# Performance work log

Hardware: AMD Instinct MI355X
Metric: run time of the kernel (lower is better)

The kernel has to match this reference:

```python
import jax, jax.numpy as jnp
import numpy as np

LN_EPS = 1e-5  # torch LayerNorm default
K_NN = 5       # top-5 nearest patterns (simple-surprise path)


def setup_inputs() -> dict:
    key = jax.random.key(0)
    ks = jax.random.split(key, 5)
    B, S, D, M = 8, 8192, 256, 50
    return {
        "hidden_states": jax.random.normal(ks[0], (B, S, D), dtype=jnp.float32),
        "memory": jax.random.normal(ks[1], (M, D), dtype=jnp.float32),
        "W1": jax.random.normal(ks[2], (D, 2 * D), dtype=jnp.float32) * (1.0 / np.sqrt(D)),
        "b1": jnp.zeros((2 * D,), dtype=jnp.float32),
        "W2": jax.random.normal(ks[3], (2 * D, D), dtype=jnp.float32) * (1.0 / np.sqrt(2 * D)),
        "b2": jnp.zeros((D,), dtype=jnp.float32),
        "ln_gamma": jnp.ones((D,), dtype=jnp.float32),
        "ln_beta": jnp.zeros((D,), dtype=jnp.float32),
    }


def reference(hidden_states, memory, W1, b1, W2, b2, ln_gamma, ln_beta):
    # Feature extractor: Linear -> ReLU -> (Dropout, eval=identity) -> Linear -> LayerNorm
    h = jax.nn.relu(jnp.einsum("bsd,de->bse", hidden_states, W1) + b1)
    f = jnp.einsum("bse,ed->bsd", h, W2) + b2
    mu = jnp.mean(f, axis=-1, keepdims=True)
    var = jnp.var(f, axis=-1, keepdims=True)
    feats = (f - mu) * jax.lax.rsqrt(var + LN_EPS) * ln_gamma + ln_beta  # [B,S,D]

    # Simple-surprise path, vectorized over all (b, s) tokens:
    # L2 distance of each token feature to every memory pattern.
    f_sq = jnp.sum(feats * feats, axis=-1)      # [B,S]
    m_sq = jnp.sum(memory * memory, axis=-1)    # [M]
    dots = jnp.einsum("bsd,md->bsm", feats, memory)  # [B,S,M]
    d2 = jnp.maximum(f_sq[..., None] + m_sq - 2.0 * dots, 0.0)
    dists = jnp.sqrt(d2)                        # [B,S,M]

    # k smallest distances -> mean -> sigmoid(avg - 1)
    neg_knn, _ = jax.lax.top_k(-dists, K_NN)    # [B,S,K]
    avg_dist = -jnp.mean(neg_knn, axis=-1)      # [B,S]
    surprise_scores = jax.nn.sigmoid(avg_dist - 1.0)
    return surprise_scores
```

## Files before the change

### kernel.cpp

```cpp
#include <hip/hip_runtime.h>
#include <math.h>

typedef __attribute__((ext_vector_type(8))) short bf16x8;
typedef __attribute__((ext_vector_type(4))) float f32x4;
typedef unsigned short ushort_t;

static __device__ __forceinline__ unsigned short f2b(float x) {
  unsigned int u = __float_as_uint(x);
  u += 0x7FFFu + ((u >> 16) & 1u);
  return (unsigned short)(u >> 16);
}

static __device__ __forceinline__ void transpose_tile(
    const float* __restrict__ src, ushort_t* __restrict__ dst, int srcC,
    int dstC, int r0, int c0, ushort_t (*T)[72], int t) {
#pragma unroll
  for (int j = 0; j < 4; ++j) {
    int idx = j * 256 + t;
    int lr = idx >> 4;
    int lc = (idx & 15) << 2;
    float4 v = *(const float4*)(&src[(size_t)(r0 + lr) * srcC + c0 + lc]);
    T[lr][lc + 0] = f2b(v.x);
    T[lr][lc + 1] = f2b(v.y);
    T[lr][lc + 2] = f2b(v.z);
    T[lr][lc + 3] = f2b(v.w);
  }
  __syncthreads();
#pragma unroll
  for (int j = 0; j < 2; ++j) {
    int oidx = j * 256 + t;
    int lc = oidx >> 3;
    int rch = (oidx & 7) << 3;
    ushort_t tmp[8];
#pragma unroll
    for (int k = 0; k < 8; ++k) tmp[k] = T[rch + k][lc];
    *(uint4*)(&dst[(size_t)(c0 + lc) * dstC + r0 + rch]) = *(uint4*)tmp;
  }
}

__global__ void prep(const float* __restrict__ W1, const float* __restrict__ W2,
                     const float* __restrict__ mem, ushort_t* __restrict__ W1T,
                     ushort_t* __restrict__ W2T, ushort_t* __restrict__ memB,
                     float* __restrict__ msq) {
  __shared__ ushort_t T[64][72];
  int b = blockIdx.x;
  int t = threadIdx.x;
  if (b < 32) {
    int tr = b >> 3, tc = b & 7;
    transpose_tile(W1, W1T, 512, 256, tr * 64, tc * 64, T, t);
  } else if (b < 64) {
    int bb = b - 32;
    int tr = bb >> 2, tc = bb & 3;
    transpose_tile(W2, W2T, 256, 512, tr * 64, tc * 64, T, t);
  } else {
    for (int i = t; i < 16384; i += 256) {
      int r = i >> 8;
      memB[i] = (r < 50) ? f2b(mem[i]) : (ushort_t)0;
    }
    int r = t >> 2, seg = t & 3;
    float s = 0.f;
    if (r < 50) {
#pragma unroll
      for (int i = 0; i < 16; i += 4) {
        float4 v = *(const float4*)(&mem[r * 256 + seg * 64 + i * 4]);
        s += v.x * v.x + v.y * v.y + v.z * v.z + v.w * v.w;
      }
    }
    s += __shfl_xor(s, 1, 64);
    s += __shfl_xor(s, 2, 64);
    if (seg == 0) msq[r] = (r < 50) ? s : 1e30f;
  }
}

#define XP 264
#define HP 136
#define DPitch 65

__global__ __launch_bounds__(256, 3) void fused_main(
    const float* __restrict__ X, const float* __restrict__ b1v,
    const float* __restrict__ b2v, const float* __restrict__ gammav,
    const float* __restrict__ betav, const ushort_t* __restrict__ W1T,
    const ushort_t* __restrict__ W2T, const ushort_t* __restrict__ memB,
    const float* __restrict__ msq, float* __restrict__ out) {
  __shared__ __align__(16) char smem[54272];
  ushort_t* Xs = (ushort_t*)smem;
  ushort_t* Hs = (ushort_t*)(smem + 33792);
  float* distS = (float*)(smem + 33792);
  float* red = (float*)(smem + 50432);
  float* psum   = red;
  float* psumsq = red + 256;
  float* fsqp   = red + 512;
  float* muS    = red + 768;
  float* rstdS  = red + 832;
  float* fsqS   = red + 896;

  const int tid = threadIdx.x;
  const int wid = tid >> 6;
  const int lane = tid & 63;
  const int l16 = lane & 15;
  const int quad = lane >> 4;

  const float4* X4 = (const float4*)(X + (size_t)blockIdx.x * 64 * 256);
#pragma unroll
  for (int j = 0; j < 16; ++j) {
    int idx = j * 256 + tid;
    float4 v = X4[idx];
    int row = idx >> 6, c4 = (idx & 63) << 2;
    unsigned int p0 = f2b(v.x) | ((unsigned int)f2b(v.y) << 16);
    unsigned int p1 = f2b(v.z) | ((unsigned int)f2b(v.w) << 16);
    *(uint2*)(&Xs[row * XP + c4]) = make_uint2(p0, p1);
  }

  f32x4 acc2[4][4];
#pragma unroll
  for (int mt = 0; mt < 4; ++mt) {
    const float4 bb = *(const float4*)(&b2v[wid * 64 + mt * 16 + quad * 4]);
#pragma unroll
    for (int nt = 0; nt < 4; ++nt) {
      acc2[mt][nt][0] = bb.x; acc2[mt][nt][1] = bb.y;
      acc2[mt][nt][2] = bb.z; acc2[mt][nt][3] = bb.w;
    }
  }

  __syncthreads();

  for (int cc = 0; cc < 4; ++cc) {
    int hbase = cc * 128 + wid * 32;
    f32x4 acc1[2][4];
#pragma unroll
    for (int mt = 0; mt < 2; ++mt) {
      const float4 bb = *(const float4*)(&b1v[hbase + mt * 16 + quad * 4]);
#pragma unroll
      for (int nt = 0; nt < 4; ++nt) {
        acc1[mt][nt][0] = bb.x; acc1[mt][nt][1] = bb.y;
        acc1[mt][nt][2] = bb.z; acc1[mt][nt][3] = bb.w;
      }
    }
#pragma unroll
    for (int kk = 0; kk < 8; ++kk) {
      int k0 = kk * 32 + quad * 8;
      bf16x8 a[2], b[4];
#pragma unroll
      for (int mt = 0; mt < 2; ++mt)
        a[mt] = *(const bf16x8*)(W1T + (hbase + mt * 16 + l16) * 256 + k0);
#pragma unroll
      for (int nt = 0; nt < 4; ++nt)
        b[nt] = *(const bf16x8*)(Xs + (nt * 16 + l16) * XP + k0);
#pragma unroll
      for (int mt = 0; mt < 2; ++mt)
#pragma unroll
        for (int nt = 0; nt < 4; ++nt)
          acc1[mt][nt] = __builtin_amdgcn_mfma_f32_16x16x32_bf16(
              a[mt], b[nt], acc1[mt][nt], 0, 0, 0);
    }
    __syncthreads();
#pragma unroll
    for (int mt = 0; mt < 2; ++mt) {
#pragma unroll
      for (int nt = 0; nt < 4; ++nt) {
        int token = nt * 16 + l16;
        int hloc = wid * 32 + mt * 16 + quad * 4;
        f32x4 v = acc1[mt][nt];
        unsigned int p0 = f2b(fmaxf(v[0], 0.f)) | ((unsigned int)f2b(fmaxf(v[1], 0.f)) << 16);
        unsigned int p1 = f2b(fmaxf(v[2], 0.f)) | ((unsigned int)f2b(fmaxf(v[3], 0.f)) << 16);
        *(uint2*)(&Hs[token * HP + hloc]) = make_uint2(p0, p1);
      }
    }
    __syncthreads();
#pragma unroll
    for (int k2 = 0; k2 < 4; ++k2) {
      int k0 = k2 * 32 + quad * 8;
      bf16x8 a[4], b[4];
#pragma unroll
      for (int mt = 0; mt < 4; ++mt)
        a[mt] = *(const bf16x8*)(W2T + (wid * 64 + mt * 16 + l16) * 512 + cc * 128 + k0);
#pragma unroll
      for (int nt = 0; nt < 4; ++nt)
        b[nt] = *(const bf16x8*)(Hs + (nt * 16 + l16) * HP + k0);
#pragma unroll
      for (int mt = 0; mt < 4; ++mt)
#pragma unroll
        for (int nt = 0; nt < 4; ++nt)
          acc2[mt][nt] = __builtin_amdgcn_mfma_f32_16x16x32_bf16(
              a[mt], b[nt], acc2[mt][nt], 0, 0, 0);
    }
  }
  __syncthreads();

#pragma unroll
  for (int nt = 0; nt < 4; ++nt) {
    float s = 0.f, sq = 0.f;
#pragma unroll
    for (int mt = 0; mt < 4; ++mt)
#pragma unroll
      for (int r = 0; r < 4; ++r) {
        float v = acc2[mt][nt][r];
        s += v; sq += v * v;
      }
    s += __shfl_xor(s, 16, 64); sq += __shfl_xor(sq, 16, 64);
    s += __shfl_xor(s, 32, 64); sq += __shfl_xor(sq, 32, 64);
    if (quad == 0) {
      psum[wid * 64 + nt * 16 + l16] = s;
      psumsq[wid * 64 + nt * 16 + l16] = sq;
    }
  }
  __syncthreads();
  if (tid < 64) {
    float s = psum[tid] + psum[64 + tid] + psum[128 + tid] + psum[192 + tid];
    float sq = psumsq[tid] + psumsq[64 + tid] + psumsq[128 + tid] + psumsq[192 + tid];
    float mu = s * (1.f / 256.f);
    float var = sq * (1.f / 256.f) - mu * mu;
    muS[tid] = mu;
    rstdS[tid] = rsqrtf(var + 1e-5f);
  }
  __syncthreads();

  {
    float4 g[4], be[4];
#pragma unroll
    for (int mt = 0; mt < 4; ++mt) {
      g[mt]  = *(const float4*)(&gammav[wid * 64 + mt * 16 + quad * 4]);
      be[mt] = *(const float4*)(&betav[wid * 64 + mt * 16 + quad * 4]);
    }
#pragma unroll
    for (int nt = 0; nt < 4; ++nt) {
      int token = nt * 16 + l16;
      float mu = muS[token], rs = rstdS[token];
      float fs = 0.f;
#pragma unroll
      for (int mt = 0; mt < 4; ++mt) {
        float y0 = (acc2[mt][nt][0] - mu) * rs * g[mt].x + be[mt].x;
        float y1 = (acc2[mt][nt][1] - mu) * rs * g[mt].y + be[mt].y;
        float y2 = (acc2[mt][nt][2] - mu) * rs * g[mt].z + be[mt].z;
        float y3 = (acc2[mt][nt][3] - mu) * rs * g[mt].w + be[mt].w;
        fs += y0 * y0 + y1 * y1 + y2 * y2 + y3 * y3;
        unsigned int p0 = f2b(y0) | ((unsigned int)f2b(y1) << 16);
        unsigned int p1 = f2b(y2) | ((unsigned int)f2b(y3) << 16);
        *(uint2*)(&Xs[token * XP + wid * 64 + mt * 16 + quad * 4]) =
            make_uint2(p0, p1);
      }
      fs += __shfl_xor(fs, 16, 64);
      fs += __shfl_xor(fs, 32, 64);
      if (quad == 0) fsqp[wid * 64 + token] = fs;
    }
  }
  __syncthreads();

  if (tid < 64)
    fsqS[tid] = fsqp[tid] + fsqp[64 + tid] + fsqp[128 + tid] + fsqp[192 + tid];

  f32x4 acc3[4];
#pragma unroll
  for (int nt = 0; nt < 4; ++nt) {
    acc3[nt][0] = 0.f; acc3[nt][1] = 0.f; acc3[nt][2] = 0.f; acc3[nt][3] = 0.f;
  }
#pragma unroll
  for (int kk = 0; kk < 8; ++kk) {
    int k0 = kk * 32 + quad * 8;
    bf16x8 a = *(const bf16x8*)(Xs + (wid * 16 + l16) * XP + k0);
#pragma unroll
    for (int nt = 0; nt < 4; ++nt) {
      bf16x8 b = *(const bf16x8*)(memB + (nt * 16 + l16) * 256 + k0);
      acc3[nt] = __builtin_amdgcn_mfma_f32_16x16x32_bf16(a, b, acc3[nt], 0, 0, 0);
    }
  }
  __syncthreads();
  {
    float4 fsq4 = *(const float4*)(&fsqS[wid * 16 + quad * 4]);
#pragma unroll
    for (int nt = 0; nt < 4; ++nt) {
      int col = nt * 16 + l16;
      float mq = msq[col];
#pragma unroll
      for (int r = 0; r < 4; ++r) {
        float fv = (r == 0) ? fsq4.x : (r == 1) ? fsq4.y : (r == 2) ? fsq4.z : fsq4.w;
        float d2 = fv + mq - 2.f * acc3[nt][r];
        float d = sqrtf(fmaxf(d2, 0.f));
        int row = wid * 16 + quad * 4 + r;
        distS[row * DPitch + col] = d;
      }
    }
  }
  __syncthreads();

  if (tid < 64) {
    float b0 = 1e30f, b1 = 1e30f, b2 = 1e30f, b3 = 1e30f, b4 = 1e30f;
    const float* dr = &distS[tid * DPitch];
    for (int j = 0; j < 50; ++j) {
      float v = dr[j];
      b4 = fminf(b4, v);
      float t;
      if (b4 < b3) { t = b3; b3 = b4; b4 = t; }
      if (b3 < b2) { t = b2; b2 = b3; b3 = t; }
      if (b2 < b1) { t = b1; b1 = b2; b2 = t; }
      if (b1 < b0) { t = b0; b0 = b1; b1 = t; }
    }
    float avg = (b0 + b1 + b2 + b3 + b4) * 0.2f;
    float sarg = avg - 1.f;
    out[blockIdx.x * 64 + tid] = 1.f / (1.f + __expf(-sarg));
  }
}

extern "C" void kernel_launch(void* const* d_in, const int* in_sizes, int n_in,
                              void* d_out, int out_size, void* d_ws, size_t ws_size,
                              hipStream_t stream) {
  const float* X   = (const float*)d_in[0];
  const float* mem = (const float*)d_in[1];
  const float* W1  = (const float*)d_in[2];
  const float* b1  = (const float*)d_in[3];
  const float* W2  = (const float*)d_in[4];
  const float* b2  = (const float*)d_in[5];
  const float* g   = (const float*)d_in[6];
  const float* be  = (const float*)d_in[7];
  float* out = (float*)d_out;

  ushort_t* W1T  = (ushort_t*)d_ws;
  ushort_t* W2T  = W1T + 131072;
  ushort_t* memB = W2T + 131072;
  float* msq = (float*)(memB + 16384);

  prep<<<65, 256, 0, stream>>>(W1, W2, mem, W1T, W2T, memB, msq);
  fused_main<<<1024, 256, 0, stream>>>(X, b1, b2, g, be, W1T, W2T, memB, msq, out);
}
```

Before: 207.7 us.

## Halve tokens per block, swizzle LDS layout, raise occupancy to five blocks

```diff
diff --git a/kernel.cpp b/kernel.cpp
--- a/kernel.cpp
+++ b/kernel.cpp
@@ -72,27 +72,22 @@
   }
 }
 
-#define XP 264
-#define HP 136
-#define DPitch 65
-
-__global__ __launch_bounds__(256, 3) void fused_main(
+__global__ __launch_bounds__(256, 5) void fused_main(
     const float* __restrict__ X, const float* __restrict__ b1v,
     const float* __restrict__ b2v, const float* __restrict__ gammav,
     const float* __restrict__ betav, const ushort_t* __restrict__ W1T,
     const ushort_t* __restrict__ W2T, const ushort_t* __restrict__ memB,
     const float* __restrict__ msq, float* __restrict__ out) {
-  __shared__ __align__(16) char smem[54272];
-  ushort_t* Xs = (ushort_t*)smem;
-  ushort_t* Hs = (ushort_t*)(smem + 33792);
-  float* distS = (float*)(smem + 33792);
-  float* red = (float*)(smem + 50432);
-  float* psum   = red;
-  float* psumsq = red + 256;
-  float* fsqp   = red + 512;
-  float* muS    = red + 768;
-  float* rstdS  = red + 832;
-  float* fsqS   = red + 896;
+  __shared__ __align__(16) char smem[25600];
+  char* Xs = smem;
+  char* Hs = smem + 16384;
+  float* distS  = (float*)(smem + 16384);
+  float* psum   = (float*)(smem + 16384);
+  float* psumsq = (float*)(smem + 16896);
+  float* fsqp   = (float*)(smem + 24704);
+  float* muS    = (float*)(smem + 25216);
+  float* rstdS  = (float*)(smem + 25344);
+  float* fsqS   = (float*)(smem + 25472);
 
   const int tid = threadIdx.x;
   const int wid = tid >> 6;
@@ -100,23 +95,26 @@
   const int l16 = lane & 15;
   const int quad = lane >> 4;
 
-  const float4* X4 = (const float4*)(X + (size_t)blockIdx.x * 64 * 256);
-#pragma unroll
-  for (int j = 0; j < 16; ++j) {
+  const float4* X4 = (const float4*)(X + (size_t)blockIdx.x * 32 * 256);
+#pragma unroll
+  for (int j = 0; j < 8; ++j) {
     int idx = j * 256 + tid;
     float4 v = X4[idx];
-    int row = idx >> 6, c4 = (idx & 63) << 2;
+    int row = idx >> 6;
+    int c = (idx & 63) >> 1;
+    int half = idx & 1;
+    int slot = c ^ (row & 7);
     unsigned int p0 = f2b(v.x) | ((unsigned int)f2b(v.y) << 16);
     unsigned int p1 = f2b(v.z) | ((unsigned int)f2b(v.w) << 16);
-    *(uint2*)(&Xs[row * XP + c4]) = make_uint2(p0, p1);
-  }
-
-  f32x4 acc2[4][4];
+    *(uint2*)(Xs + row * 512 + slot * 16 + half * 8) = make_uint2(p0, p1);
+  }
+
+  f32x4 acc2[4][2];
 #pragma unroll
   for (int mt = 0; mt < 4; ++mt) {
     const float4 bb = *(const float4*)(&b2v[wid * 64 + mt * 16 + quad * 4]);
 #pragma unroll
-    for (int nt = 0; nt < 4; ++nt) {
+    for (int nt = 0; nt < 2; ++nt) {
       acc2[mt][nt][0] = bb.x; acc2[mt][nt][1] = bb.y;
       acc2[mt][nt][2] = bb.z; acc2[mt][nt][3] = bb.w;
     }
@@ -126,12 +124,12 @@
 
   for (int cc = 0; cc < 4; ++cc) {
     int hbase = cc * 128 + wid * 32;
-    f32x4 acc1[2][4];
+    f32x4 acc1[2][2];
 #pragma unroll
     for (int mt = 0; mt < 2; ++mt) {
       const float4 bb = *(const float4*)(&b1v[hbase + mt * 16 + quad * 4]);
 #pragma unroll
-      for (int nt = 0; nt < 4; ++nt) {
+      for (int nt = 0; nt < 2; ++nt) {
         acc1[mt][nt][0] = bb.x; acc1[mt][nt][1] = bb.y;
         acc1[mt][nt][2] = bb.z; acc1[mt][nt][3] = bb.w;
       }
@@ -139,17 +137,20 @@
 #pragma unroll
     for (int kk = 0; kk < 8; ++kk) {
       int k0 = kk * 32 + quad * 8;
-      bf16x8 a[2], b[4];
+      bf16x8 a[2], b[2];
 #pragma unroll
       for (int mt = 0; mt < 2; ++mt)
         a[mt] = *(const bf16x8*)(W1T + (hbase + mt * 16 + l16) * 256 + k0);
-#pragma unroll
-      for (int nt = 0; nt < 4; ++nt)
-        b[nt] = *(const bf16x8*)(Xs + (nt * 16 + l16) * XP + k0);
+      int c = kk * 4 + quad;
+#pragma unroll
+      for (int nt = 0; nt < 2; ++nt) {
+        int t = nt * 16 + l16;
+        b[nt] = *(const bf16x8*)(Xs + t * 512 + (c ^ (t & 7)) * 16);
+      }
 #pragma unroll
       for (int mt = 0; mt < 2; ++mt)
 #pragma unroll
-        for (int nt = 0; nt < 4; ++nt)
+        for (int nt = 0; nt < 2; ++nt)
           acc1[mt][nt] = __builtin_amdgcn_mfma_f32_16x16x32_bf16(
               a[mt], b[nt], acc1[mt][nt], 0, 0, 0);
     }
@@ -157,30 +158,37 @@
 #pragma unroll
     for (int mt = 0; mt < 2; ++mt) {
 #pragma unroll
-      for (int nt = 0; nt < 4; ++nt) {
+      for (int nt = 0; nt < 2; ++nt) {
         int token = nt * 16 + l16;
         int hloc = wid * 32 + mt * 16 + quad * 4;
+        int c = wid * 4 + mt * 2 + (quad >> 1);
+        int half = quad & 1;
+        int slot = c ^ (token & 7);
         f32x4 v = acc1[mt][nt];
         unsigned int p0 = f2b(fmaxf(v[0], 0.f)) | ((unsigned int)f2b(fmaxf(v[1], 0.f)) << 16);
         unsigned int p1 = f2b(fmaxf(v[2], 0.f)) | ((unsigned int)f2b(fmaxf(v[3], 0.f)) << 16);
-        *(uint2*)(&Hs[token * HP + hloc]) = make_uint2(p0, p1);
+        *(uint2*)(Hs + token * 256 + slot * 16 + half * 8) = make_uint2(p0, p1);
+        (void)hloc;
       }
     }
     __syncthreads();
 #pragma unroll
     for (int k2 = 0; k2 < 4; ++k2) {
-      int k0 = k2 * 32 + quad * 8;
-      bf16x8 a[4], b[4];
+      int c = k2 * 4 + quad;
+      bf16x8 a[4], b[2];
 #pragma unroll
       for (int mt = 0; mt < 4; ++mt)
-        a[mt] = *(const bf16x8*)(W2T + (wid * 64 + mt * 16 + l16) * 512 + cc * 128 + k0);
-#pragma unroll
-      for (int nt = 0; nt < 4; ++nt)
-        b[nt] = *(const bf16x8*)(Hs + (nt * 16 + l16) * HP + k0);
+        a[mt] = *(const bf16x8*)(W2T + (wid * 64 + mt * 16 + l16) * 512 +
+                                 cc * 128 + k2 * 32 + quad * 8);
+#pragma unroll
+      for (int nt = 0; nt < 2; ++nt) {
+        int t = nt * 16 + l16;
+        b[nt] = *(const bf16x8*)(Hs + t * 256 + (c ^ (t & 7)) * 16);
+      }
 #pragma unroll
       for (int mt = 0; mt < 4; ++mt)
 #pragma unroll
-        for (int nt = 0; nt < 4; ++nt)
+        for (int nt = 0; nt < 2; ++nt)
           acc2[mt][nt] = __builtin_amdgcn_mfma_f32_16x16x32_bf16(
               a[mt], b[nt], acc2[mt][nt], 0, 0, 0);
     }
@@ -188,7 +196,7 @@
   __syncthreads();
 
 #pragma unroll
-  for (int nt = 0; nt < 4; ++nt) {
+  for (int nt = 0; nt < 2; ++nt) {
     float s = 0.f, sq = 0.f;
 #pragma unroll
     for (int mt = 0; mt < 4; ++mt)
@@ -200,14 +208,14 @@
     s += __shfl_xor(s, 16, 64); sq += __shfl_xor(sq, 16, 64);
     s += __shfl_xor(s, 32, 64); sq += __shfl_xor(sq, 32, 64);
     if (quad == 0) {
-      psum[wid * 64 + nt * 16 + l16] = s;
-      psumsq[wid * 64 + nt * 16 + l16] = sq;
-    }
-  }
-  __syncthreads();
-  if (tid < 64) {
-    float s = psum[tid] + psum[64 + tid] + psum[128 + tid] + psum[192 + tid];
-    float sq = psumsq[tid] + psumsq[64 + tid] + psumsq[128 + tid] + psumsq[192 + tid];
+      psum[wid * 32 + nt * 16 + l16] = s;
+      psumsq[wid * 32 + nt * 16 + l16] = sq;
+    }
+  }
+  __syncthreads();
+  if (tid < 32) {
+    float s = psum[tid] + psum[32 + tid] + psum[64 + tid] + psum[96 + tid];
+    float sq = psumsq[tid] + psumsq[32 + tid] + psumsq[64 + tid] + psumsq[96 + tid];
     float mu = s * (1.f / 256.f);
     float var = sq * (1.f / 256.f) - mu * mu;
     muS[tid] = mu;
@@ -223,7 +231,7 @@
       be[mt] = *(const float4*)(&betav[wid * 64 + mt * 16 + quad * 4]);
     }
 #pragma unroll
-    for (int nt = 0; nt < 4; ++nt) {
+    for (int nt = 0; nt < 2; ++nt) {
       int token = nt * 16 + l16;
       float mu = muS[token], rs = rstdS[token];
       float fs = 0.f;
@@ -234,58 +242,64 @@
         float y2 = (acc2[mt][nt][2] - mu) * rs * g[mt].z + be[mt].z;
         float y3 = (acc2[mt][nt][3] - mu) * rs * g[mt].w + be[mt].w;
         fs += y0 * y0 + y1 * y1 + y2 * y2 + y3 * y3;
+        int c = wid * 8 + mt * 2 + (quad >> 1);
+        int half = quad & 1;
+        int slot = c ^ (token & 7);
         unsigned int p0 = f2b(y0) | ((unsigned int)f2b(y1) << 16);
         unsigned int p1 = f2b(y2) | ((unsigned int)f2b(y3) << 16);
-        *(uint2*)(&Xs[token * XP + wid * 64 + mt * 16 + quad * 4]) =
-            make_uint2(p0, p1);
+        *(uint2*)(Xs + token * 512 + slot * 16 + half * 8) = make_uint2(p0, p1);
       }
       fs += __shfl_xor(fs, 16, 64);
       fs += __shfl_xor(fs, 32, 64);
-      if (quad == 0) fsqp[wid * 64 + token] = fs;
-    }
-  }
-  __syncthreads();
-
-  if (tid < 64)
-    fsqS[tid] = fsqp[tid] + fsqp[64 + tid] + fsqp[128 + tid] + fsqp[192 + tid];
-
-  f32x4 acc3[4];
-#pragma unroll
-  for (int nt = 0; nt < 4; ++nt) {
+      if (quad == 0) fsqp[wid * 32 + token] = fs;
+    }
+  }
+  __syncthreads();
+
+  if (tid < 32)
+    fsqS[tid] = fsqp[tid] + fsqp[32 + tid] + fsqp[64 + tid] + fsqp[96 + tid];
+
+  const int th = wid & 1;
+  const int mh = wid >> 1;
+  f32x4 acc3[2];
+#pragma unroll
+  for (int nt = 0; nt < 2; ++nt) {
     acc3[nt][0] = 0.f; acc3[nt][1] = 0.f; acc3[nt][2] = 0.f; acc3[nt][3] = 0.f;
   }
 #pragma unroll
   for (int kk = 0; kk < 8; ++kk) {
-    int k0 = kk * 32 + quad * 8;
-    bf16x8 a = *(const bf16x8*)(Xs + (wid * 16 + l16) * XP + k0);
-#pragma unroll
-    for (int nt = 0; nt < 4; ++nt) {
-      bf16x8 b = *(const bf16x8*)(memB + (nt * 16 + l16) * 256 + k0);
+    int c = kk * 4 + quad;
+    int t = th * 16 + l16;
+    bf16x8 a = *(const bf16x8*)(Xs + t * 512 + (c ^ (t & 7)) * 16);
+#pragma unroll
+    for (int nt = 0; nt < 2; ++nt) {
+      int mrow = mh * 32 + nt * 16 + l16;
+      bf16x8 b = *(const bf16x8*)(memB + mrow * 256 + kk * 32 + quad * 8);
       acc3[nt] = __builtin_amdgcn_mfma_f32_16x16x32_bf16(a, b, acc3[nt], 0, 0, 0);
     }
   }
   __syncthreads();
   {
-    float4 fsq4 = *(const float4*)(&fsqS[wid * 16 + quad * 4]);
-#pragma unroll
-    for (int nt = 0; nt < 4; ++nt) {
-      int col = nt * 16 + l16;
+    float4 fsq4 = *(const float4*)(&fsqS[th * 16 + quad * 4]);
+#pragma unroll
+    for (int nt = 0; nt < 2; ++nt) {
+      int col = mh * 32 + nt * 16 + l16;
       float mq = msq[col];
 #pragma unroll
       for (int r = 0; r < 4; ++r) {
         float fv = (r == 0) ? fsq4.x : (r == 1) ? fsq4.y : (r == 2) ? fsq4.z : fsq4.w;
         float d2 = fv + mq - 2.f * acc3[nt][r];
         float d = sqrtf(fmaxf(d2, 0.f));
-        int row = wid * 16 + quad * 4 + r;
-        distS[row * DPitch + col] = d;
-      }
-    }
-  }
-  __syncthreads();
-
-  if (tid < 64) {
+        int row = th * 16 + quad * 4 + r;
+        distS[row * 65 + col] = d;
+      }
+    }
+  }
+  __syncthreads();
+
+  if (tid < 32) {
     float b0 = 1e30f, b1 = 1e30f, b2 = 1e30f, b3 = 1e30f, b4 = 1e30f;
-    const float* dr = &distS[tid * DPitch];
+    const float* dr = &distS[tid * 65];
     for (int j = 0; j < 50; ++j) {
       float v = dr[j];
       b4 = fminf(b4, v);
@@ -296,8 +310,7 @@
       if (b1 < b0) { t = b0; b0 = b1; b1 = t; }
     }
     float avg = (b0 + b1 + b2 + b3 + b4) * 0.2f;
-    float sarg = avg - 1.f;
-    out[blockIdx.x * 64 + tid] = 1.f / (1.f + __expf(-sarg));
+    out[blockIdx.x * 32 + tid] = 1.f / (1.f + __expf(-(avg - 1.f)));
   }
 }
 
@@ -320,5 +333,5 @@
   float* msq = (float*)(memB + 16384);
 
   prep<<<65, 256, 0, stream>>>(W1, W2, mem, W1T, W2T, memB, msq);
-  fused_main<<<1024, 256, 0, stream>>>(X, b1, b2, g, be, W1T, W2T, memB, msq, out);
-}
+  fused_main<<<2048, 256, 0, stream>>>(X, b1, b2, g, be, W1T, W2T, memB, msq, out);
+}
```

Measured after the change: 276.4 us. 33.1% more time.

## Swizzle LDS tiles and prefetch weight fragments into registers

Applied to the files above, without the earlier changes.

```diff
diff --git a/kernel.cpp b/kernel.cpp
--- a/kernel.cpp
+++ b/kernel.cpp
@@ -72,27 +72,22 @@
   }
 }
 
-#define XP 264
-#define HP 136
-#define DPitch 65
-
-__global__ __launch_bounds__(256, 3) void fused_main(
+__global__ __launch_bounds__(256, 2) void fused_main(
     const float* __restrict__ X, const float* __restrict__ b1v,
     const float* __restrict__ b2v, const float* __restrict__ gammav,
     const float* __restrict__ betav, const ushort_t* __restrict__ W1T,
     const ushort_t* __restrict__ W2T, const ushort_t* __restrict__ memB,
     const float* __restrict__ msq, float* __restrict__ out) {
-  __shared__ __align__(16) char smem[54272];
-  ushort_t* Xs = (ushort_t*)smem;
-  ushort_t* Hs = (ushort_t*)(smem + 33792);
-  float* distS = (float*)(smem + 33792);
-  float* red = (float*)(smem + 50432);
-  float* psum   = red;
-  float* psumsq = red + 256;
-  float* fsqp   = red + 512;
-  float* muS    = red + 768;
-  float* rstdS  = red + 832;
-  float* fsqS   = red + 896;
+  __shared__ __align__(16) char smem[50176];
+  char* Xs = smem;
+  char* Hs = smem + 32768;
+  float* distS  = (float*)(smem + 32768);
+  float* psum   = (float*)(smem + 32768);
+  float* psumsq = (float*)(smem + 33792);
+  float* fsqp   = (float*)(smem + 34816);
+  float* muS    = (float*)(smem + 49408);
+  float* rstdS  = (float*)(smem + 49664);
+  float* fsqS   = (float*)(smem + 49920);
 
   const int tid = threadIdx.x;
   const int wid = tid >> 6;
@@ -100,15 +95,28 @@
   const int l16 = lane & 15;
   const int quad = lane >> 4;
 
+  bf16x8 w1f[2][8];
+  {
+    int hbase = wid * 32;
+#pragma unroll
+    for (int mt = 0; mt < 2; ++mt)
+#pragma unroll
+      for (int kk = 0; kk < 8; ++kk)
+        w1f[mt][kk] = *(const bf16x8*)(W1T + (hbase + mt * 16 + l16) * 256 +
+                                       kk * 32 + quad * 8);
+  }
+
   const float4* X4 = (const float4*)(X + (size_t)blockIdx.x * 64 * 256);
 #pragma unroll
   for (int j = 0; j < 16; ++j) {
     int idx = j * 256 + tid;
     float4 v = X4[idx];
-    int row = idx >> 6, c4 = (idx & 63) << 2;
+    int row = idx >> 6;
+    int f = idx & 63;
+    int slot = (f >> 1) ^ (row & 7);
     unsigned int p0 = f2b(v.x) | ((unsigned int)f2b(v.y) << 16);
     unsigned int p1 = f2b(v.z) | ((unsigned int)f2b(v.w) << 16);
-    *(uint2*)(&Xs[row * XP + c4]) = make_uint2(p0, p1);
+    *(uint2*)(Xs + row * 512 + slot * 16 + (f & 1) * 8) = make_uint2(p0, p1);
   }
 
   f32x4 acc2[4][4];
@@ -138,51 +146,66 @@
     }
 #pragma unroll
     for (int kk = 0; kk < 8; ++kk) {
-      int k0 = kk * 32 + quad * 8;
-      bf16x8 a[2], b[4];
-#pragma unroll
-      for (int mt = 0; mt < 2; ++mt)
-        a[mt] = *(const bf16x8*)(W1T + (hbase + mt * 16 + l16) * 256 + k0);
-#pragma unroll
-      for (int nt = 0; nt < 4; ++nt)
-        b[nt] = *(const bf16x8*)(Xs + (nt * 16 + l16) * XP + k0);
+      int c = kk * 4 + quad;
+      bf16x8 b[4];
+#pragma unroll
+      for (int nt = 0; nt < 4; ++nt) {
+        int t = nt * 16 + l16;
+        b[nt] = *(const bf16x8*)(Xs + t * 512 + ((c ^ (t & 7)) << 4));
+      }
 #pragma unroll
       for (int mt = 0; mt < 2; ++mt)
 #pragma unroll
         for (int nt = 0; nt < 4; ++nt)
           acc1[mt][nt] = __builtin_amdgcn_mfma_f32_16x16x32_bf16(
-              a[mt], b[nt], acc1[mt][nt], 0, 0, 0);
-    }
+              w1f[mt][kk], b[nt], acc1[mt][nt], 0, 0, 0);
+    }
+    bf16x8 w2f[4][4];
+#pragma unroll
+    for (int mt = 0; mt < 4; ++mt)
+#pragma unroll
+      for (int k2 = 0; k2 < 4; ++k2)
+        w2f[mt][k2] = *(const bf16x8*)(W2T + (wid * 64 + mt * 16 + l16) * 512 +
+                                       cc * 128 + k2 * 32 + quad * 8);
     __syncthreads();
 #pragma unroll
     for (int mt = 0; mt < 2; ++mt) {
 #pragma unroll
       for (int nt = 0; nt < 4; ++nt) {
         int token = nt * 16 + l16;
-        int hloc = wid * 32 + mt * 16 + quad * 4;
+        int c = wid * 4 + mt * 2 + (quad >> 1);
+        int slot = c ^ (token & 7);
         f32x4 v = acc1[mt][nt];
         unsigned int p0 = f2b(fmaxf(v[0], 0.f)) | ((unsigned int)f2b(fmaxf(v[1], 0.f)) << 16);
         unsigned int p1 = f2b(fmaxf(v[2], 0.f)) | ((unsigned int)f2b(fmaxf(v[3], 0.f)) << 16);
-        *(uint2*)(&Hs[token * HP + hloc]) = make_uint2(p0, p1);
+        *(uint2*)(Hs + token * 256 + slot * 16 + (quad & 1) * 8) = make_uint2(p0, p1);
       }
     }
     __syncthreads();
+    if (cc < 3) {
+      int hb = (cc + 1) * 128 + wid * 32;
+#pragma unroll
+      for (int mt = 0; mt < 2; ++mt)
+#pragma unroll
+        for (int kk = 0; kk < 8; ++kk)
+          w1f[mt][kk] = *(const bf16x8*)(W1T + (hb + mt * 16 + l16) * 256 +
+                                         kk * 32 + quad * 8);
+    }
 #pragma unroll
     for (int k2 = 0; k2 < 4; ++k2) {
-      int k0 = k2 * 32 + quad * 8;
-      bf16x8 a[4], b[4];
-#pragma unroll
-      for (int mt = 0; mt < 4; ++mt)
-        a[mt] = *(const bf16x8*)(W2T + (wid * 64 + mt * 16 + l16) * 512 + cc * 128 + k0);
-#pragma unroll
-      for (int nt = 0; nt < 4; ++nt)
-        b[nt] = *(const bf16x8*)(Hs + (nt * 16 + l16) * HP + k0);
+      int c = k2 * 4 + quad;
+      bf16x8 b[4];
+#pragma unroll
+      for (int nt = 0; nt < 4; ++nt) {
+        int t = nt * 16 + l16;
+        b[nt] = *(const bf16x8*)(Hs + t * 256 + ((c ^ (t & 7)) << 4));
+      }
 #pragma unroll
       for (int mt = 0; mt < 4; ++mt)
 #pragma unroll
         for (int nt = 0; nt < 4; ++nt)
           acc2[mt][nt] = __builtin_amdgcn_mfma_f32_16x16x32_bf16(
-              a[mt], b[nt], acc2[mt][nt], 0, 0, 0);
+              w2f[mt][k2], b[nt], acc2[mt][nt], 0, 0, 0);
     }
   }
   __syncthreads();
@@ -234,10 +257,11 @@
         float y2 = (acc2[mt][nt][2] - mu) * rs * g[mt].z + be[mt].z;
         float y3 = (acc2[mt][nt][3] - mu) * rs * g[mt].w + be[mt].w;
         fs += y0 * y0 + y1 * y1 + y2 * y2 + y3 * y3;
+        int c = wid * 8 + mt * 2 + (quad >> 1);
+        int slot = c ^ (token & 7);
         unsigned int p0 = f2b(y0) | ((unsigned int)f2b(y1) << 16);
         unsigned int p1 = f2b(y2) | ((unsigned int)f2b(y3) << 16);
-        *(uint2*)(&Xs[token * XP + wid * 64 + mt * 16 + quad * 4]) =
-            make_uint2(p0, p1);
+        *(uint2*)(Xs + token * 512 + slot * 16 + (quad & 1) * 8) = make_uint2(p0, p1);
       }
       fs += __shfl_xor(fs, 16, 64);
       fs += __shfl_xor(fs, 32, 64);
@@ -249,20 +273,25 @@
   if (tid < 64)
     fsqS[tid] = fsqp[tid] + fsqp[64 + tid] + fsqp[128 + tid] + fsqp[192 + tid];
 
+  bf16x8 mf[4][8];
+#pragma unroll
+  for (int nt = 0; nt < 4; ++nt)
+#pragma unroll
+    for (int kk = 0; kk < 8; ++kk)
+      mf[nt][kk] = *(const bf16x8*)(memB + (nt * 16 + l16) * 256 + kk * 32 + quad * 8);
   f32x4 acc3[4];
 #pragma unroll
   for (int nt = 0; nt < 4; ++nt) {
     acc3[nt][0] = 0.f; acc3[nt][1] = 0.f; acc3[nt][2] = 0.f; acc3[nt][3] = 0.f;
   }
+  const int t3 = wid * 16 + l16;
 #pragma unroll
   for (int kk = 0; kk < 8; ++kk) {
-    int k0 = kk * 32 + quad * 8;
-    bf16x8 a = *(const bf16x8*)(Xs + (wid * 16 + l16) * XP + k0);
-#pragma unroll
-    for (int nt = 0; nt < 4; ++nt) {
-      bf16x8 b = *(const bf16x8*)(memB + (nt * 16 + l16) * 256 + k0);
-      acc3[nt] = __builtin_amdgcn_mfma_f32_16x16x32_bf16(a, b, acc3[nt], 0, 0, 0);
-    }
+    int c = kk * 4 + quad;
+    bf16x8 a = *(const bf16x8*)(Xs + t3 * 512 + ((c ^ (t3 & 7)) << 4));
+#pragma unroll
+    for (int nt = 0; nt < 4; ++nt)
+      acc3[nt] = __builtin_amdgcn_mfma_f32_16x16x32_bf16(a, mf[nt][kk], acc3[nt], 0, 0, 0);
   }
   __syncthreads();
   {
@@ -277,7 +306,7 @@
         float d2 = fv + mq - 2.f * acc3[nt][r];
         float d = sqrtf(fmaxf(d2, 0.f));
         int row = wid * 16 + quad * 4 + r;
-        distS[row * DPitch + col] = d;
+        distS[row * 65 + col] = d;
       }
     }
   }
@@ -285,7 +314,7 @@
 
   if (tid < 64) {
     float b0 = 1e30f, b1 = 1e30f, b2 = 1e30f, b3 = 1e30f, b4 = 1e30f;
-    const float* dr = &distS[tid * DPitch];
+    const float* dr = &distS[tid * 65];
     for (int j = 0; j < 50; ++j) {
       float v = dr[j];
       b4 = fminf(b4, v);
@@ -296,8 +325,7 @@
       if (b1 < b0) { t = b0; b0 = b1; b1 = t; }
     }
     float avg = (b0 + b1 + b2 + b3 + b4) * 0.2f;
-    float sarg = avg - 1.f;
-    out[blockIdx.x * 64 + tid] = 1.f / (1.f + __expf(-sarg));
+    out[blockIdx.x * 64 + tid] = 1.f / (1.f + __expf(-(avg - 1.f)));
   }
 }
 
```

Result: faster. 201.1 us (-3.2%).
